# Kernel tuning notes

Hardware: AMD Instinct MI355X
Metric: run time of the kernel (lower is better)

Reference implementation:

```python
import jax, jax.numpy as jnp
import numpy as np

CUTOFF = 3.0   # self.cutoff
RMIN = 3.5     # rmin in cutoff_function (note rmin > cutoff, faithful to source)
ETA = 4.0
N_RADIAL = 5
N_3BODY = 12
NATOMS = 2048
K = 48         # neighbors per atom (equal counts -> ragged loop becomes dense batch)
HID = 64
NPAIRS = NATOMS * K


def setup_inputs() -> dict:
    key = jax.random.key(0)
    ks = jax.random.split(key, 4)
    # displacements scaled so |rij| is mostly within a few Angstrom
    rij = jax.random.normal(ks[0], (NPAIRS, 3), jnp.float32) * 1.5
    # sorted-by-atom pair list with K neighbors per atom
    unique_i = jnp.repeat(jnp.arange(NATOMS, dtype=jnp.int64), K)
    W1 = jax.random.normal(ks[1], (N_RADIAL + N_3BODY, HID), jnp.float32) * 0.1
    b1 = jnp.zeros((HID,), jnp.float32)
    W2 = jax.random.normal(ks[2], (HID, HID), jnp.float32) * 0.1
    b2 = jnp.zeros((HID,), jnp.float32)
    W3 = jax.random.normal(ks[3], (HID, 1), jnp.float32) * 0.1
    b3 = jnp.zeros((1,), jnp.float32)
    return dict(rij=rij, unique_i=unique_i, W1=W1, b1=b1, W2=W2, b2=b2, W3=W3, b3=b3)


def _energy(rij, W1, b1, W2, b2, W3, b3):
    d = jnp.linalg.norm(rij, axis=1, keepdims=True)           # (P,1)
    diff_norm = rij / jnp.maximum(d, 1e-12)                   # F.normalize
    # pair cutoff (rmin=3.5, c=3.0 as in source)
    fc = jnp.where(d > RMIN,
                   0.5 + 0.5 * jnp.cos(jnp.pi * (d - RMIN) / (CUTOFF - RMIN)),
                   1.0)
    # radial Bessel basis, n = 1..5
    ns = jnp.arange(1, N_RADIAL + 1, dtype=rij.dtype)
    rbf = jnp.sqrt(2.0 / CUTOFF) * jnp.sin(ns * jnp.pi / CUTOFF * d) / d * fc  # (P,5)
    # 3-body Gaussian descriptors
    fcrik = (0.5 + 0.5 * jnp.cos(jnp.pi * d / CUTOFF))[:, 0]  # (P,)
    dn = diff_norm.reshape(NATOMS, K, 3)
    cosang = jnp.einsum('nkd,nld->nkl', dn, dn)               # (N,K,K) pairwise mm
    cosang = jnp.where(jnp.eye(K, dtype=bool)[None], 0.0, cosang)  # fill_diagonal_(0)
    mu = jnp.linspace(-1.0, 1.0, N_3BODY).astype(rij.dtype)
    w = fcrik.reshape(NATOMS, 1, K, 1)                        # fcrik broadcast on axis being summed
    g3b = jnp.sum(jnp.exp(-ETA * (cosang[..., None] - mu) ** 2) * w, axis=2)  # (N,K,12)
    g3b = g3b.reshape(NPAIRS, N_3BODY)
    desc = jnp.concatenate([rbf, g3b], axis=1)                # (P,17)
    h = jnp.tanh(desc @ W1 + b1)
    h = jnp.tanh(h @ W2 + b2)
    eij = h @ W3 + b3                                         # (P,1)
    return jnp.sum(eij * fc)


def reference(rij, unique_i, W1, b1, W2, b2, W3, b3):
    # Module output: gradients of total energy w.r.t. rij (written into beta)
    return jax.grad(_energy)(rij, W1, b1, W2, b2, W3, b3)
```

## Files before the change

### kernel.cpp

```cpp
#include <hip/hip_runtime.h>
#include <hip/hip_bf16.h>

#define NATOMS 2048
#define K 48
#define P (NATOMS * K)
#define NR 5
#define NM 12
#define ND 17
#define HID 64

#define PI_F 3.14159265358979f
#define CUT 3.0f
#define RMIN_F 3.5f
#define AFC (-6.28318530717959f)
#define POC (PI_F / CUT)
#define SQ 0.816496580927726f
#define E1C 1.45454545454545f
#define CMC (-0.132231404958678f)

__device__ unsigned short g_w1t[64 * 32];
__device__ unsigned short g_w2t[64 * 64];
__device__ unsigned short g_w2r[64 * 64];
__device__ unsigned short g_w1r[32 * 64];

using frag_ab = __attribute__((ext_vector_type(8))) short;
using frag_cd = __attribute__((ext_vector_type(4))) float;

__device__ __forceinline__ float fast_tanh(float x) {
    float cx = fminf(fmaxf(x, -15.0f), 15.0f);
    float t = __expf(2.0f * cx);
    return (t - 1.0f) / (t + 1.0f);
}

__device__ __forceinline__ unsigned short f2bs(float x) {
    __hip_bfloat16 b = __float2bfloat16(x);
    return __builtin_bit_cast(unsigned short, b);
}

__global__ __launch_bounds__(256) void k_prep(const float* __restrict__ W1,
                                              const float* __restrict__ W2) {
    const int i = blockIdx.x * 256 + threadIdx.x;
    if (i < 2048) {
        const int n = i >> 5, k = i & 31;
        g_w1t[i] = (k < ND) ? f2bs(W1[k * HID + n]) : (unsigned short)0;
    } else if (i < 2048 + 4096) {
        const int j = i - 2048, n = j >> 6, k = j & 63;
        g_w2t[j] = f2bs(W2[k * HID + n]);
    } else if (i < 2048 + 8192) {
        const int j = i - (2048 + 4096);
        g_w2r[j] = f2bs(W2[j]);
    } else if (i < 2048 + 8192 + 2048) {
        const int j = i - (2048 + 8192), n = j >> 6;
        g_w1r[j] = (n < ND) ? f2bs(W1[j]) : (unsigned short)0;
    }
}

#define SC_OFF    0
#define H1_OFF    9408
#define GZ2_OFF   16320
#define DESC_OFF  23232
#define SGD_OFF   27072
#define SU_OFF    30720
#define SFC_OFF   31296
#define SFK_OFF   31488
#define SD_OFF    31680
#define SM_BYTES  31872
#define SPART_OFF 9408
#define SGG_OFF   9408
#define SGU_OFF   11712
#define SGF_OFF   12288
#define ST_OFF    16320
#define SE_OFF    23232

__global__ __launch_bounds__(256, 5) void k_fused(const float* __restrict__ rij,
                                                  const float* __restrict__ b1,
                                                  const float* __restrict__ b2,
                                                  const float* __restrict__ W3,
                                                  const float* __restrict__ b3,
                                                  float* __restrict__ out) {
    __shared__ __align__(16) char smem[SM_BYTES];
    float* sc    = (float*)(smem + SC_OFF);
    short* h1S   = (short*)(smem + H1_OFF);
    short* gz2S  = (short*)(smem + GZ2_OFF);
    short* descS = (short*)(smem + DESC_OFF);
    float* spart = (float*)(smem + SPART_OFF);
    float* sgG   = (float*)(smem + SGG_OFF);
    float* sT    = (float*)(smem + ST_OFF);
    float* sgd   = (float*)(smem + SGD_OFF);
    float* su    = (float*)(smem + SU_OFF);
    float* sfc   = (float*)(smem + SFC_OFF);
    float* sfk   = (float*)(smem + SFK_OFF);
    float* sd    = (float*)(smem + SD_OFF);
    float* se    = (float*)(smem + SE_OFF);
    float* sgf   = (float*)(smem + SGF_OFF);
    float* sgu   = (float*)(smem + SGU_OFF);

    const int t = threadIdx.x;
    const int base3 = blockIdx.x * (K * 3);

    if (t < K) {
        const float x = rij[base3 + 3 * t];
        const float y = rij[base3 + 3 * t + 1];
        const float z = rij[base3 + 3 * t + 2];
        const float d = sqrtf(x * x + y * y + z * z);
        const float inv = 1.0f / fmaxf(d, 1e-12f);
        su[3 * t] = x * inv; su[3 * t + 1] = y * inv; su[3 * t + 2] = z * inv;
        sd[t] = d;
        sfk[t] = 0.5f + 0.5f * __cosf(POC * d);
        const float fc = (d > RMIN_F) ? (0.5f + 0.5f * __cosf(AFC * (d - RMIN_F))) : 1.0f;
        sfc[t] = fc;
        const float s = SQ * fc / d;
#pragma unroll
        for (int n = 0; n < NR; n++) {
            const float bn = (float)(n + 1) * POC;
            descS[t * 40 + n] = (short)f2bs(s * __sinf(bn * d));
        }
#pragma unroll
        for (int c = ND; c < 32; c++) descS[t * 40 + c] = 0;
    }
    __syncthreads();

    for (int idx = t; idx < K * K; idx += 256) {
        const int k = idx / K, l = idx - k * K;
        const float c = su[3 * k] * su[3 * l] + su[3 * k + 1] * su[3 * l + 1]
                      + su[3 * k + 2] * su[3 * l + 2];
        sc[k * 49 + l] = (k == l) ? 0.0f : c;
    }
    __syncthreads();

    if (t < 192) {
        const int ch = t / 48, k = t - ch * 48;
        float part[NM];
#pragma unroll
        for (int m = 0; m < NM; m++) part[m] = 0.0f;
#pragma unroll
        for (int li = 0; li < 12; li++) {
            const int l = ch * 12 + li;
            const float cp1 = sc[k * 49 + l] + 1.0f;
            const float e0 = __expf(-4.0f * cp1 * cp1) * sfk[l];
            const float e1 = __expf(E1C * cp1);
            float tm = e0;
            part[0] += tm;
#pragma unroll
            for (int m = 1; m < NM; m++) { tm *= e1; part[m] += tm; }
        }
#pragma unroll
        for (int m = 0; m < NM; m++) spart[(ch * 48 + k) * 13 + m] = part[m];
    }
    __syncthreads();

    for (int idx = t; idx < K * NM; idx += 256) {
        const int k = idx / NM, m = idx - k * NM;
        const float cm = __expf(CMC * (float)(m * m));
        const float s = spart[(0 * 48 + k) * 13 + m] + spart[(1 * 48 + k) * 13 + m]
                      + spart[(2 * 48 + k) * 13 + m] + spart[(3 * 48 + k) * 13 + m];
        descS[k * 40 + NR + m] = (short)f2bs(s * cm);
    }
    __syncthreads();

    const int w = t >> 6, lane = t & 63, quad = lane >> 4, lm = lane & 15;
    const int n0 = w * 16 + lm;

    float t1[3][4];
    {
        const frag_ab bf = *(const frag_ab*)&g_w1t[n0 * 32 + quad * 8];
        const float bias = b1[n0];
#pragma unroll
        for (int mt = 0; mt < 3; mt++) {
            const frag_ab a = *(const frag_ab*)&descS[(mt * 16 + lm) * 40 + quad * 8];
            frag_cd acc = {bias, bias, bias, bias};
            acc = __builtin_amdgcn_mfma_f32_16x16x32_bf16(a, bf, acc, 0, 0, 0);
#pragma unroll
            for (int r = 0; r < 4; r++) {
                const float tv = fast_tanh(acc[r]);
                t1[mt][r] = tv;
                h1S[(mt * 16 + quad * 4 + r) * 72 + n0] = (short)f2bs(tv);
            }
        }
    }
    __syncthreads();

    {
        const frag_ab b0 = *(const frag_ab*)&g_w2t[n0 * 64 + quad * 8];
        const frag_ab b1f = *(const frag_ab*)&g_w2t[n0 * 64 + 32 + quad * 8];
        const float bias = b2[n0];
        const float w3n = W3[n0];
#pragma unroll
        for (int mt = 0; mt < 3; mt++) {
            const frag_ab a0 = *(const frag_ab*)&h1S[(mt * 16 + lm) * 72 + quad * 8];
            const frag_ab a1 = *(const frag_ab*)&h1S[(mt * 16 + lm) * 72 + 32 + quad * 8];
            frag_cd acc = {bias, bias, bias, bias};
            acc = __builtin_amdgcn_mfma_f32_16x16x32_bf16(a0, b0, acc, 0, 0, 0);
            acc = __builtin_amdgcn_mfma_f32_16x16x32_bf16(a1, b1f, acc, 0, 0, 0);
            float ep[4];
#pragma unroll
            for (int r = 0; r < 4; r++) {
                const int row = mt * 16 + quad * 4 + r;
                const float tv = fast_tanh(acc[r]);
                ep[r] = tv * w3n;
                gz2S[row * 72 + n0] = (short)f2bs(sfc[row] * w3n * (1.0f - tv * tv));
            }
#pragma unroll
            for (int off = 1; off < 16; off <<= 1) {
#pragma unroll
                for (int r = 0; r < 4; r++) ep[r] += __shfl_xor(ep[r], off, 64);
            }
            if (lm == 0) {
#pragma unroll
                for (int r = 0; r < 4; r++) se[w * 48 + mt * 16 + quad * 4 + r] = ep[r];
            }
        }
    }
    __syncthreads();

    {
        const frag_ab b0 = *(const frag_ab*)&g_w2r[n0 * 64 + quad * 8];
        const frag_ab b1f = *(const frag_ab*)&g_w2r[n0 * 64 + 32 + quad * 8];
#pragma unroll
        for (int mt = 0; mt < 3; mt++) {
            const frag_ab a0 = *(const frag_ab*)&gz2S[(mt * 16 + lm) * 72 + quad * 8];
            const frag_ab a1 = *(const frag_ab*)&gz2S[(mt * 16 + lm) * 72 + 32 + quad * 8];
            frag_cd acc = {0.0f, 0.0f, 0.0f, 0.0f};
            acc = __builtin_amdgcn_mfma_f32_16x16x32_bf16(a0, b0, acc, 0, 0, 0);
            acc = __builtin_amdgcn_mfma_f32_16x16x32_bf16(a1, b1f, acc, 0, 0, 0);
#pragma unroll
            for (int r = 0; r < 4; r++) {
                const float g = acc[r] * (1.0f - t1[mt][r] * t1[mt][r]);
                h1S[(mt * 16 + quad * 4 + r) * 72 + n0] = (short)f2bs(g);
            }
        }
    }
    __syncthreads();

    for (int tid = w; tid < 6; tid += 4) {
        const int mt = tid >> 1, nt = tid & 1, n = nt * 16 + lm;
        const frag_ab b0 = *(const frag_ab*)&g_w1r[n * 64 + quad * 8];
        const frag_ab b1f = *(const frag_ab*)&g_w1r[n * 64 + 32 + quad * 8];
        const frag_ab a0 = *(const frag_ab*)&h1S[(mt * 16 + lm) * 72 + quad * 8];
        const frag_ab a1 = *(const frag_ab*)&h1S[(mt * 16 + lm) * 72 + 32 + quad * 8];
        frag_cd acc = {0.0f, 0.0f, 0.0f, 0.0f};
        acc = __builtin_amdgcn_mfma_f32_16x16x32_bf16(a0, b0, acc, 0, 0, 0);
        acc = __builtin_amdgcn_mfma_f32_16x16x32_bf16(a1, b1f, acc, 0, 0, 0);
        if (n < ND) {
#pragma unroll
            for (int r = 0; r < 4; r++)
                sgd[(mt * 16 + quad * 4 + r) * 19 + n] = acc[r];
        }
    }
    if (t < K)
        sgd[t * 19 + 17] = se[t] + se[48 + t] + se[96 + t] + se[144 + t] + b3[0];
    __syncthreads();

    for (int idx = t; idx < K * NM; idx += 256) {
        const int k = idx / NM, m = idx - k * NM;
        sgG[idx] = sgd[k * 19 + NR + m] * __expf(CMC * (float)(m * m));
    }
    __syncthreads();

    for (int idx = t; idx < K * K; idx += 256) {
        const int k = idx / K, l = idx - k * K;
        const float cp1 = sc[k * 49 + l] + 1.0f;
        const float e0 = __expf(-4.0f * cp1 * cp1);
        const float e1 = __expf(E1C * cp1);
        float tm = e0;
        float T = sgG[k * 12] * tm, U = 0.0f;
#pragma unroll
        for (int m = 1; m < NM; m++) {
            tm *= e1;
            const float q = sgG[k * 12 + m] * tm;
            T += q;
            U = fmaf((float)m, q, U);
        }
        const float Sp = cp1 * T - (2.0f / 11.0f) * U;
        sT[k * 48 + l] = T;
        sc[k * 49 + l] = (k == l) ? 0.0f : (-8.0f) * Sp;
    }
    __syncthreads();

    if (t < K) {
        float s = 0.0f;
#pragma unroll 4
        for (int kk = 0; kk < K; kk++) s += sT[kk * 48 + t];
        sgf[t] = s;
    } else if (t >= 64 && t < 64 + K) {
        const int k = t - 64;
        const float fk = sfk[k];
        float gx = 0.0f, gy = 0.0f, gz = 0.0f;
#pragma unroll 4
        for (int l = 0; l < K; l++) {
            const float wgt = fmaf(sc[k * 49 + l], sfk[l], sc[l * 49 + k] * fk);
            gx = fmaf(wgt, su[3 * l], gx);
            gy = fmaf(wgt, su[3 * l + 1], gy);
            gz = fmaf(wgt, su[3 * l + 2], gz);
        }
        sgu[3 * k] = gx; sgu[3 * k + 1] = gy; sgu[3 * k + 2] = gz;
    }
    __syncthreads();

    if (t < K) {
        const float d = sd[t];
        const float ux = su[3 * t], uy = su[3 * t + 1], uz = su[3 * t + 2];
        const float invd = 1.0f / d;
        float gfc = sgd[t * 19 + 17];
        float gdR = 0.0f;
#pragma unroll
        for (int n = 0; n < NR; n++) {
            const float bn = (float)(n + 1) * POC;
            float sn, cn;
            __sincosf(bn * d, &sn, &cn);
            const float g = sgd[t * 19 + n];
            gfc = fmaf(g, SQ * sn * invd, gfc);
            gdR = fmaf(g, SQ * (bn * cn - sn * invd) * invd, gdR);
        }
        const float fc = sfc[t];
        float dfc = 0.0f;
        if (d > RMIN_F) dfc = -0.5f * AFC * __sinf(AFC * (d - RMIN_F));
        const float dfcrik = -0.5f * POC * __sinf(POC * d);

        const float gd = fc * gdR + gfc * dfc + sgf[t] * dfcrik;
        const float gux = sgu[3 * t], guy = sgu[3 * t + 1], guz = sgu[3 * t + 2];
        const float dot = gux * ux + guy * uy + guz * uz;

        out[base3 + 3 * t + 0] = fmaf(gd, ux, (gux - dot * ux) * invd);
        out[base3 + 3 * t + 1] = fmaf(gd, uy, (guy - dot * uy) * invd);
        out[base3 + 3 * t + 2] = fmaf(gd, uz, (guz - dot * uz) * invd);
    }
}

extern "C" void kernel_launch(void* const* d_in, const int* in_sizes, int n_in,
                              void* d_out, int out_size, void* d_ws, size_t ws_size,
                              hipStream_t stream) {
    (void)in_sizes; (void)n_in; (void)out_size; (void)d_ws; (void)ws_size;
    const float* rij = (const float*)d_in[0];
    const float* W1 = (const float*)d_in[2];
    const float* b1 = (const float*)d_in[3];
    const float* W2 = (const float*)d_in[4];
    const float* b2 = (const float*)d_in[5];
    const float* W3 = (const float*)d_in[6];
    const float* b3 = (const float*)d_in[7];
    float* out = (float*)d_out;

    k_prep<<<48, 256, 0, stream>>>(W1, W2);
    k_fused<<<NATOMS, 256, 0, stream>>>(rij, b1, b2, W3, b3, out);
}
```

Measured before the change: 102.4 us.

## Spread backward angular and reduction phases across all warps, Horner-evaluate Gaussian sums

Moves the radial-basis descriptor computation onto otherwise idle threads 192-255 during the angular forward pass, and precomputes the per-m Gaussian constants once in shared memory. The backward angular pass now has 192 threads each handle 12 neighbors with weights held in registers, evaluating the 12-term sums as Horner polynomials. The final column-sum and gradient-vector reductions are split across all four warps and then combined. This is meant to cut serial per-thread work and idle lanes in the phases where only 48-64 threads were active, at the cost of extra shared memory, more register pressure and a final reduction step.

```diff
diff --git a/kernel.cpp b/kernel.cpp
--- a/kernel.cpp
+++ b/kernel.cpp
@@ -64,12 +64,14 @@
 #define SFC_OFF   31296
 #define SFK_OFF   31488
 #define SD_OFF    31680
-#define SM_BYTES  31872
+#define SCM_OFF   31872
+#define SM_BYTES  31920
 #define SPART_OFF 9408
 #define SGG_OFF   9408
-#define SGU_OFF   11712
-#define SGF_OFF   12288
+#define MGG_OFF   11712
+#define SGU4_OFF  14016
 #define ST_OFF    16320
+#define SGF4_OFF  25536
 #define SE_OFF    23232
 
 __global__ __launch_bounds__(256, 5) void k_fused(const float* __restrict__ rij,
@@ -85,15 +87,17 @@
     short* descS = (short*)(smem + DESC_OFF);
     float* spart = (float*)(smem + SPART_OFF);
     float* sgG   = (float*)(smem + SGG_OFF);
+    float* mgG   = (float*)(smem + MGG_OFF);
     float* sT    = (float*)(smem + ST_OFF);
     float* sgd   = (float*)(smem + SGD_OFF);
     float* su    = (float*)(smem + SU_OFF);
     float* sfc   = (float*)(smem + SFC_OFF);
     float* sfk   = (float*)(smem + SFK_OFF);
     float* sd    = (float*)(smem + SD_OFF);
+    float* scm   = (float*)(smem + SCM_OFF);
     float* se    = (float*)(smem + SE_OFF);
-    float* sgf   = (float*)(smem + SGF_OFF);
-    float* sgu   = (float*)(smem + SGU_OFF);
+    float* sgf4  = (float*)(smem + SGF4_OFF);
+    float* sgu4  = (float*)(smem + SGU4_OFF);
 
     const int t = threadIdx.x;
     const int base3 = blockIdx.x * (K * 3);
@@ -107,16 +111,13 @@
         su[3 * t] = x * inv; su[3 * t + 1] = y * inv; su[3 * t + 2] = z * inv;
         sd[t] = d;
         sfk[t] = 0.5f + 0.5f * __cosf(POC * d);
-        const float fc = (d > RMIN_F) ? (0.5f + 0.5f * __cosf(AFC * (d - RMIN_F))) : 1.0f;
-        sfc[t] = fc;
-        const float s = SQ * fc / d;
-#pragma unroll
-        for (int n = 0; n < NR; n++) {
-            const float bn = (float)(n + 1) * POC;
-            descS[t * 40 + n] = (short)f2bs(s * __sinf(bn * d));
-        }
+        sfc[t] = (d > RMIN_F) ? (0.5f + 0.5f * __cosf(AFC * (d - RMIN_F))) : 1.0f;
 #pragma unroll
         for (int c = ND; c < 32; c++) descS[t * 40 + c] = 0;
+    }
+    if (t >= 64 && t < 64 + NM) {
+        const int m = t - 64;
+        scm[m] = __expf(CMC * (float)(m * m));
     }
     __syncthreads();
 
@@ -146,15 +147,25 @@
         }
 #pragma unroll
         for (int m = 0; m < NM; m++) spart[(ch * 48 + k) * 13 + m] = part[m];
+    } else {
+#pragma unroll
+        for (int r = 0; r < 4; r++) {
+            const int idx = (t - 192) + 64 * r;
+            if (idx < K * NR) {
+                const int p = idx / NR, n = idx - NR * p;
+                const float d = sd[p];
+                const float s = SQ * sfc[p] / d;
+                descS[p * 40 + n] = (short)f2bs(s * __sinf((float)(n + 1) * POC * d));
+            }
+        }
     }
     __syncthreads();
 
     for (int idx = t; idx < K * NM; idx += 256) {
         const int k = idx / NM, m = idx - k * NM;
-        const float cm = __expf(CMC * (float)(m * m));
         const float s = spart[(0 * 48 + k) * 13 + m] + spart[(1 * 48 + k) * 13 + m]
                       + spart[(2 * 48 + k) * 13 + m] + spart[(3 * 48 + k) * 13 + m];
-        descS[k * 40 + NR + m] = (short)f2bs(s * cm);
+        descS[k * 40 + NR + m] = (short)f2bs(s * scm[m]);
     }
     __syncthreads();
 
@@ -253,51 +264,70 @@
 
     for (int idx = t; idx < K * NM; idx += 256) {
         const int k = idx / NM, m = idx - k * NM;
-        sgG[idx] = sgd[k * 19 + NR + m] * __expf(CMC * (float)(m * m));
-    }
-    __syncthreads();
-
-    for (int idx = t; idx < K * K; idx += 256) {
-        const int k = idx / K, l = idx - k * K;
-        const float cp1 = sc[k * 49 + l] + 1.0f;
-        const float e0 = __expf(-4.0f * cp1 * cp1);
-        const float e1 = __expf(E1C * cp1);
-        float tm = e0;
-        float T = sgG[k * 12] * tm, U = 0.0f;
-#pragma unroll
-        for (int m = 1; m < NM; m++) {
-            tm *= e1;
-            const float q = sgG[k * 12 + m] * tm;
-            T += q;
-            U = fmaf((float)m, q, U);
-        }
-        const float Sp = cp1 * T - (2.0f / 11.0f) * U;
-        sT[k * 48 + l] = T;
-        sc[k * 49 + l] = (k == l) ? 0.0f : (-8.0f) * Sp;
-    }
-    __syncthreads();
-
-    if (t < K) {
+        const float g = sgd[k * 19 + NR + m] * scm[m];
+        sgG[idx] = g;
+        mgG[idx] = (float)m * g;
+    }
+    __syncthreads();
+
+    if (t < 192) {
+        const int ch = t / 48, k = t - ch * 48;
+        float gg[NM], mg[NM];
+#pragma unroll
+        for (int m = 0; m < NM; m++) { gg[m] = sgG[k * 12 + m]; mg[m] = mgG[k * 12 + m]; }
+#pragma unroll
+        for (int li = 0; li < 12; li++) {
+            const int l = ch * 12 + li;
+            const float cp1 = sc[k * 49 + l] + 1.0f;
+            const float e0 = __expf(-4.0f * cp1 * cp1);
+            const float x = __expf(E1C * cp1);
+            float Pv = gg[11], Dv = mg[11];
+#pragma unroll
+            for (int m = 10; m >= 1; m--) {
+                Pv = fmaf(Pv, x, gg[m]);
+                Dv = fmaf(Dv, x, mg[m]);
+            }
+            Pv = fmaf(Pv, x, gg[0]);
+            const float T = e0 * Pv;
+            const float U = e0 * x * Dv;
+            const float Sp = fmaf(cp1, T, -(2.0f / 11.0f) * U);
+            sT[k * 48 + l] = T;
+            sc[k * 49 + l] = (k == l) ? 0.0f : (-8.0f) * Sp;
+        }
+    }
+    __syncthreads();
+
+    if (lane < K) {
         float s = 0.0f;
-#pragma unroll 4
-        for (int kk = 0; kk < K; kk++) s += sT[kk * 48 + t];
-        sgf[t] = s;
-    } else if (t >= 64 && t < 64 + K) {
-        const int k = t - 64;
+#pragma unroll
+        for (int kk = 12 * w; kk < 12 * w + 12; kk++) s += sT[kk * 48 + lane];
+        sgf4[w * 48 + lane] = s;
+
+        const int k = lane;
         const float fk = sfk[k];
         float gx = 0.0f, gy = 0.0f, gz = 0.0f;
-#pragma unroll 4
-        for (int l = 0; l < K; l++) {
+#pragma unroll
+        for (int l = 12 * w; l < 12 * w + 12; l++) {
             const float wgt = fmaf(sc[k * 49 + l], sfk[l], sc[l * 49 + k] * fk);
             gx = fmaf(wgt, su[3 * l], gx);
             gy = fmaf(wgt, su[3 * l + 1], gy);
             gz = fmaf(wgt, su[3 * l + 2], gz);
         }
-        sgu[3 * k] = gx; sgu[3 * k + 1] = gy; sgu[3 * k + 2] = gz;
+        sgu4[(w * 48 + k) * 3 + 0] = gx;
+        sgu4[(w * 48 + k) * 3 + 1] = gy;
+        sgu4[(w * 48 + k) * 3 + 2] = gz;
     }
     __syncthreads();
 
     if (t < K) {
+        const float sgf_t = sgf4[t] + sgf4[48 + t] + sgf4[96 + t] + sgf4[144 + t];
+        float gux = 0.0f, guy = 0.0f, guz = 0.0f;
+#pragma unroll
+        for (int ww = 0; ww < 4; ww++) {
+            gux += sgu4[(ww * 48 + t) * 3 + 0];
+            guy += sgu4[(ww * 48 + t) * 3 + 1];
+            guz += sgu4[(ww * 48 + t) * 3 + 2];
+        }
         const float d = sd[t];
         const float ux = su[3 * t], uy = su[3 * t + 1], uz = su[3 * t + 2];
         const float invd = 1.0f / d;
@@ -317,8 +347,7 @@
         if (d > RMIN_F) dfc = -0.5f * AFC * __sinf(AFC * (d - RMIN_F));
         const float dfcrik = -0.5f * POC * __sinf(POC * d);
 
-        const float gd = fc * gdR + gfc * dfc + sgf[t] * dfcrik;
-        const float gux = sgu[3 * t], guy = sgu[3 * t + 1], guz = sgu[3 * t + 2];
+        const float gd = fc * gdR + gfc * dfc + sgf_t * dfcrik;
         const float dot = gux * ux + guy * uy + guz * uz;
 
         out[base3 + 3 * t + 0] = fmaf(gd, ux, (gux - dot * ux) * invd);
```

New measurement: 101.4 us. About the same (-0.9%).
